# Kernel optimization log

Hardware: AMD Instinct MI355X
Metric: run time of the kernel (lower is better)

## Reference

```python
import jax, jax.numpy as jnp
import numpy as np

D = 1024  # image side length (input_shape[-1])
K = 3     # kernel_dim
B = 64    # batch


def setup_inputs() -> dict:
    key = jax.random.key(0)
    k1, k2 = jax.random.split(key)
    inputs = jax.random.normal(k1, (B, D * D), dtype=jnp.float32)
    kernel = jax.random.normal(k2, (K, K), dtype=jnp.float32)
    return {"inputs": inputs, "kernel": kernel}


def reference(inputs, kernel):
    # Original builds a dense [O^2, D^2] Toeplitz matrix from the kernel and
    # does y = (M @ inputs^T)^T. That is exactly a VALID 2D cross-correlation
    # of each flattened image with the [K,K] kernel.
    b = inputs.shape[0]
    img = inputs.reshape(b, 1, D, D)            # NCHW
    w = kernel.reshape(1, 1, K, K)              # OIHW
    out = jax.lax.conv_general_dilated(
        img, w, window_strides=(1, 1), padding="VALID",
        dimension_numbers=("NCHW", "OIHW", "NCHW"))
    o = D - K + 1
    return out.reshape(b, o * o)
```

## Files before the change

kernel.cpp:

```cpp
#include <hip/hip_runtime.h>

#define D_IMG 1024
#define K_DIM 3
#define O_IMG 1022
#define RPT   8

__global__ __launch_bounds__(256) void conv3x3_kernel(
    const float* __restrict__ in,
    const float* __restrict__ w,
    float* __restrict__ out)
{
    const int strips_per_img = (O_IMG + RPT - 1) / RPT;
    const int bid   = blockIdx.x;
    const int img   = bid / strips_per_img;
    const int strip = bid % strips_per_img;
    const int y0    = strip * RPT;
    const int x0    = threadIdx.x * 4;

    const float* ip = in  + (size_t)img * (D_IMG * D_IMG);
    float*       op = out + (size_t)img * ((size_t)O_IMG * O_IMG);

    const float k00 = w[0], k01 = w[1], k02 = w[2];
    const float k10 = w[3], k11 = w[4], k12 = w[5];
    const float k20 = w[6], k21 = w[7], k22 = w[8];

    const bool tail = (x0 + 8 > D_IMG);

    float r[3][8];

    auto loadrow = [&](int y, float* dst) {
        const float4 a = *(const float4*)(ip + (size_t)y * D_IMG + x0);
        dst[0] = a.x; dst[1] = a.y; dst[2] = a.z; dst[3] = a.w;
        if (!tail) {
            const float4 b = *(const float4*)(ip + (size_t)y * D_IMG + x0 + 4);
            dst[4] = b.x; dst[5] = b.y; dst[6] = b.z; dst[7] = b.w;
        } else {
            dst[4] = dst[5] = dst[6] = dst[7] = 0.f;
        }
    };

    loadrow(y0,     r[0]);
    loadrow(y0 + 1, r[1]);

    #pragma unroll
    for (int i = 0; i < RPT; ++i) {
        const int y = y0 + i;
        if (y >= O_IMG) break;
        loadrow(y + 2, r[(i + 2) % 3]);

        const float* a = r[(i + 0) % 3];
        const float* b = r[(i + 1) % 3];
        const float* c = r[(i + 2) % 3];

        float acc[4];
        #pragma unroll
        for (int j = 0; j < 4; ++j) {
            acc[j] = a[j] * k00 + a[j+1] * k01 + a[j+2] * k02
                   + b[j] * k10 + b[j+1] * k11 + b[j+2] * k12
                   + c[j] * k20 + c[j+1] * k21 + c[j+2] * k22;
        }

        float* orow = op + (size_t)y * O_IMG + x0;
        if (!tail) {
            *(float2*)(orow + 0) = make_float2(acc[0], acc[1]);
            *(float2*)(orow + 2) = make_float2(acc[2], acc[3]);
        } else {
            orow[0] = acc[0];
            orow[1] = acc[1];
        }
    }
}

extern "C" void kernel_launch(void* const* d_in, const int* in_sizes, int n_in,
                              void* d_out, int out_size, void* d_ws, size_t ws_size,
                              hipStream_t stream) {
    const float* in = (const float*)d_in[0];
    const float* w  = (const float*)d_in[1];
    float* out      = (float*)d_out;

    const int B = 64;
    const int strips_per_img = (O_IMG + RPT - 1) / RPT;
    dim3 grid(B * strips_per_img);
    dim3 block(256);
    conv3x3_kernel<<<grid, block, 0, stream>>>(in, w, out);
}
```

Measured before the change: 456.5 us.

## Remap blocks across XCDs, enlarge strips, and trim per-thread row loads

Workgroup IDs are remapped so that consecutive strips of an image land on the same XCD, which should improve L2 reuse of the halo rows shared between strips. The strip height rises to 14 rows so that 73 strips cover 1022 rows exactly, which removes the row bounds check and cuts the halo reload overhead. Each thread now loads 6 floats (a float4 plus a float2) instead of 8. The last thread's x offset is clamped so the tail branches go away; it overlaps and redundantly writes the same values as its neighbour.

```diff
diff --git a/kernel.cpp b/kernel.cpp
--- a/kernel.cpp
+++ b/kernel.cpp
@@ -1,42 +1,43 @@
 #include <hip/hip_runtime.h>
 
-#define D_IMG 1024
-#define K_DIM 3
-#define O_IMG 1022
-#define RPT   8
+#define D_IMG  1024
+#define K_DIM  3
+#define O_IMG  1022
+#define RPT    14
+#define STRIPS 73
+#define NXCD   8
 
 __global__ __launch_bounds__(256) void conv3x3_kernel(
     const float* __restrict__ in,
     const float* __restrict__ w,
     float* __restrict__ out)
 {
-    const int strips_per_img = (O_IMG + RPT - 1) / RPT;
-    const int bid   = blockIdx.x;
-    const int img   = bid / strips_per_img;
-    const int strip = bid % strips_per_img;
+    int bid = blockIdx.x;
+    {
+        const int nwg = 64 * STRIPS;
+        const int cpx = nwg / NXCD;
+        bid = (bid % NXCD) * cpx + bid / NXCD;
+    }
+    const int img   = bid / STRIPS;
+    const int strip = bid % STRIPS;
     const int y0    = strip * RPT;
-    const int x0    = threadIdx.x * 4;
+    const int x0    = min((int)threadIdx.x * 4, O_IMG - 4);
 
-    const float* ip = in  + (size_t)img * (D_IMG * D_IMG);
+    const float* ip = in  + (size_t)img * ((size_t)D_IMG * D_IMG);
     float*       op = out + (size_t)img * ((size_t)O_IMG * O_IMG);
 
     const float k00 = w[0], k01 = w[1], k02 = w[2];
     const float k10 = w[3], k11 = w[4], k12 = w[5];
     const float k20 = w[6], k21 = w[7], k22 = w[8];
 
-    const bool tail = (x0 + 8 > D_IMG);
-
-    float r[3][8];
+    float r[3][6];
 
     auto loadrow = [&](int y, float* dst) {
-        const float4 a = *(const float4*)(ip + (size_t)y * D_IMG + x0);
+        const float* p = ip + (size_t)y * D_IMG + x0;
+        const float4 a = *(const float4*)(p);
+        const float2 b = *(const float2*)(p + 4);
         dst[0] = a.x; dst[1] = a.y; dst[2] = a.z; dst[3] = a.w;
-        if (!tail) {
-            const float4 b = *(const float4*)(ip + (size_t)y * D_IMG + x0 + 4);
-            dst[4] = b.x; dst[5] = b.y; dst[6] = b.z; dst[7] = b.w;
-        } else {
-            dst[4] = dst[5] = dst[6] = dst[7] = 0.f;
-        }
+        dst[4] = b.x; dst[5] = b.y;
     };
 
     loadrow(y0,     r[0]);
@@ -45,7 +46,6 @@
     #pragma unroll
     for (int i = 0; i < RPT; ++i) {
         const int y = y0 + i;
-        if (y >= O_IMG) break;
         loadrow(y + 2, r[(i + 2) % 3]);
 
         const float* a = r[(i + 0) % 3];
@@ -61,13 +61,8 @@
         }
 
         float* orow = op + (size_t)y * O_IMG + x0;
-        if (!tail) {
-            *(float2*)(orow + 0) = make_float2(acc[0], acc[1]);
-            *(float2*)(orow + 2) = make_float2(acc[2], acc[3]);
-        } else {
-            orow[0] = acc[0];
-            orow[1] = acc[1];
-        }
+        *(float2*)(orow + 0) = make_float2(acc[0], acc[1]);
+        *(float2*)(orow + 2) = make_float2(acc[2], acc[3]);
     }
 }
 
@@ -79,8 +74,7 @@
     float* out      = (float*)d_out;
 
     const int B = 64;
-    const int strips_per_img = (O_IMG + RPT - 1) / RPT;
-    dim3 grid(B * strips_per_img);
+    dim3 grid(B * STRIPS);
     dim3 block(256);
     conv3x3_kernel<<<grid, block, 0, stream>>>(in, w, out);
 }
```

New measurement: 433.7 us. 1.05x faster.
